# Performance work log

Measured on AMD Instinct MI355X. Metric: run time of the kernel, lower is better.

## Reference

```python
import jax, jax.numpy as jnp
import numpy as np

NUM_GRAPHS = 1024
NODES_PER_GRAPH = 1024
HIDDEN = 128
RANK_K = 8


def _mlp(x, w1, b1, w2, b2):
    # Linear -> ReLU -> Linear
    return jax.nn.relu(x @ w1 + b1) @ w2 + b2


def setup_inputs() -> dict:
    key = jax.random.key(0)
    ks = jax.random.split(key, 13)
    N = NUM_GRAPHS * NODES_PER_GRAPH
    H = jax.random.normal(ks[0], (N, HIDDEN), dtype=jnp.float32)
    # equal-size graphs: sorted graph ids 0..G-1, each repeated n_per times
    batch = jnp.repeat(jnp.arange(NUM_GRAPHS, dtype=jnp.int32), NODES_PER_GRAPH)
    s = 0.05
    p = {
        "d_w1": jax.random.normal(ks[1], (HIDDEN, HIDDEN)) * s,
        "d_b1": jnp.zeros((HIDDEN,), jnp.float32),
        "d_w2": jax.random.normal(ks[2], (HIDDEN, 2)) * s,
        "d_b2": jnp.zeros((2,), jnp.float32),
        "u_w1": jax.random.normal(ks[3], (HIDDEN, HIDDEN)) * s,
        "u_b1": jnp.zeros((HIDDEN,), jnp.float32),
        "u_w2": jax.random.normal(ks[4], (HIDDEN, 2 * RANK_K)) * s,
        "u_b2": jnp.zeros((2 * RANK_K,), jnp.float32),
        "s_w1": jax.random.normal(ks[5], (HIDDEN, HIDDEN)) * s,
        "s_b1": jnp.zeros((HIDDEN,), jnp.float32),
        "s_w2": jax.random.normal(ks[6], (HIDDEN, RANK_K)) * s,
        "s_b2": jnp.zeros((RANK_K,), jnp.float32),
    }
    return {"H": H, "batch": batch, **p}


def reference(H, batch, d_w1, d_b1, d_w2, d_b2, u_w1, u_b1, u_w2, u_b2, s_w1, s_b1, s_w2, s_b2):
    # per-node heads
    d_raw = _mlp(H, d_w1, d_b1, d_w2, d_b2)            # [N, 2]
    u_raw = _mlp(H, u_w1, u_b1, u_w2, u_b2)            # [N, 2k]
    # global_mean_pool: segment mean over graph ids
    sums = jax.ops.segment_sum(H, batch, num_segments=NUM_GRAPHS)          # [G, d]
    counts = jax.ops.segment_sum(jnp.ones((H.shape[0],), H.dtype), batch,
                                 num_segments=NUM_GRAPHS)                   # [G]
    h_pool = sums / counts[:, None]
    s_raw = _mlp(h_pool, s_w1, s_b1, s_w2, s_b2)       # [G, k]
    d_all = jax.nn.softplus(d_raw)
    s_all = jax.nn.softplus(s_raw)
    # equal-sized graphs -> the per-graph ragged gather+reshape is a pure reshape
    n = NODES_PER_GRAPH
    d = d_all.reshape(NUM_GRAPHS, 2 * n)               # per-graph d_g [2n]
    U = u_raw.reshape(NUM_GRAPHS, 2 * n, RANK_K)       # per-graph U_g [2n, k]
    return (d, U, s_all)
```

## Files before the change

kernel.cpp:

```cpp
#include <hip/hip_runtime.h>
#include <hip/hip_bf16.h>

#define G_NUM 1024
#define NPG   1024
#define HID   128
#define TILE_ROWS 32
#define TILES_PER_WG 32
#define GRAPHS_PER_WG 1

typedef __attribute__((ext_vector_type(8))) short   short8;
typedef __attribute__((ext_vector_type(4))) float   floatx4;

__device__ __forceinline__ unsigned short f2bf(float f) {
  unsigned int u = __float_as_uint(f);
  u += 0x7fffu + ((u >> 16) & 1u);
  return (unsigned short)(u >> 16);
}

__device__ __forceinline__ unsigned int cvt_pk_bf16(float lo, float hi) {
  unsigned int r;
  asm("v_cvt_pk_bf16_f32 %0, %1, %2" : "=v"(r) : "v"(lo), "v"(hi));
  return r;
}

__device__ __forceinline__ void wg_barrier_lds() {
  asm volatile("s_waitcnt lgkmcnt(0)\n\ts_barrier" ::: "memory");
}

__device__ __forceinline__ float softplusf(float x) {
  float t = exp2f(-fabsf(x) * 1.44269504f);
  return fmaxf(x, 0.f) + 0.69314718f * log2f(1.f + t);
}

__global__ void prep_kernel(const float* __restrict__ d_w1, const float* __restrict__ d_b1,
                            const float* __restrict__ d_w2,
                            const float* __restrict__ u_w1, const float* __restrict__ u_b1,
                            const float* __restrict__ u_w2,
                            const float* __restrict__ d_b2, const float* __restrict__ u_b2,
                            unsigned short* __restrict__ Wt1, unsigned short* __restrict__ W2t,
                            float* __restrict__ b1cat, float* __restrict__ b2cat)
{
  int id = blockIdx.x * blockDim.x + threadIdx.x;
  int stride = gridDim.x * blockDim.x;
  for (int idx = id; idx < 32768; idx += stride) {
    int c = idx >> 7, k = idx & 127;
    float v = (c < 128) ? d_w1[k * 128 + c] : u_w1[k * 128 + (c - 128)];
    Wt1[idx] = f2bf(v);
  }
  for (int idx = id; idx < 8192; idx += stride) {
    int c2 = idx >> 8, h = idx & 255;
    float v = 0.f;
    if (h < 128) { if (c2 < 2) v = d_w2[h * 2 + c2]; }
    else         { if (c2 >= 2 && c2 < 18) v = u_w2[(h - 128) * 16 + (c2 - 2)]; }
    W2t[idx] = f2bf(v);
  }
  for (int idx = id; idx < 256; idx += stride)
    b1cat[idx] = (idx < 128) ? d_b1[idx] : u_b1[idx - 128];
  for (int idx = id; idx < 32; idx += stride)
    b2cat[idx] = (idx < 2) ? d_b2[idx] : ((idx < 18) ? u_b2[idx - 2] : 0.f);
}

__global__ __launch_bounds__(256, 2) void fused_kernel(
    const float* __restrict__ H,
    const unsigned short* __restrict__ Wt1, const unsigned short* __restrict__ W2t,
    const float* __restrict__ b1cat, const float* __restrict__ b2cat,
    const float* __restrict__ s_w1, const float* __restrict__ s_b1,
    const float* __restrict__ s_w2, const float* __restrict__ s_b2,
    float* __restrict__ out)
{
  __shared__ __align__(16) unsigned short sH0 [TILE_ROWS * 128];
  __shared__ __align__(16) unsigned short sH1 [TILE_ROWS * 128];
  __shared__ __align__(16) unsigned short sC1a[TILE_ROWS * 256];
  __shared__ __align__(16) unsigned short sC1b[TILE_ROWS * 256];
  __shared__ __align__(16) float sX[768];

  const int tid  = threadIdx.x;
  const int g    = blockIdx.x;
  const int lane = tid & 63;
  const int w    = tid >> 6;
  const int l15  = lane & 15;
  const int l4   = lane >> 4;

  float* outD = out;
  float* outU = out + 2097152;
  float* outS = out + 18874368;

  short8 b1f[4][4];
  float  b1b[4];
#pragma unroll
  for (int nt = 0; nt < 4; ++nt) {
    int c = 64 * w + 16 * nt + l15;
    b1b[nt] = b1cat[c];
#pragma unroll
    for (int ks = 0; ks < 4; ++ks)
      b1f[nt][ks] = *(const short8*)(Wt1 + c * 128 + 32 * ks + 8 * l4);
  }
  const int r0 = 16 * (w >> 1);
  const int c0 = 16 * (w & 1);
  short8 w2f[8];
#pragma unroll
  for (int s8 = 0; s8 < 8; ++s8)
    w2f[s8] = *(const short8*)(W2t + (c0 + l15) * 256 + 32 * s8 + 8 * l4);
  const float b2v = b2cat[c0 + l15];

  const unsigned selw = (l15 & 1) ? 0x03020706u : 0x05040100u;
  const bool hi2 = (l15 & 2) != 0;

  const float* Hb = H + (long)g * (NPG * HID);

  float4 psum = make_float4(0.f, 0.f, 0.f, 0.f);

  float4 svA[4], svB[4];
#pragma unroll
  for (int i = 0; i < 4; ++i) svA[i] = *(const float4*)(Hb + i * 1024 + tid * 4);
#pragma unroll
  for (int i = 0; i < 4; ++i) svB[i] = *(const float4*)(Hb + 4096 + i * 1024 + tid * 4);

  auto regionC = [&](const unsigned short* sCr, int tc) {
    floatx4 acc2 = {b2v, b2v, b2v, b2v};
#pragma unroll
    for (int s8 = 0; s8 < 8; ++s8) {
      int r = r0 + l15;
      int bo = r * 512 + 64 * s8 + 16 * l4;
      bo ^= (r & 7) << 4;
      short8 a2 = *(const short8*)((const char*)sCr + bo);
      acc2 = __builtin_amdgcn_mfma_f32_16x16x32_bf16(a2, w2f[s8], acc2, 0, 0, 0);
    }
    long nodebase = (long)g * NPG + tc * TILE_ROWS + r0 + 4 * l4;
    if (c0 == 0) {
#pragma unroll
      for (int q = 0; q < 4; ++q) {
        float v = acc2[q];
        long node = nodebase + q;
        if (l15 < 2) outD[node * 2 + l15] = softplusf(v);
        else         outU[node * 16 + (l15 - 2)] = v;
      }
    } else {
#pragma unroll
      for (int q = 0; q < 4; ++q) {
        long node = nodebase + q;
        if (l15 < 2) outU[node * 16 + 14 + l15] = acc2[q];
      }
    }
  };

  auto body = [&](float4 (&cur)[4], unsigned short* sHw,
                  const unsigned short* sCr, unsigned short* sCw, int t) {
#pragma unroll
    for (int i = 0; i < 4; ++i) {
      float4 v = cur[i];
      psum.x += v.x; psum.y += v.y; psum.z += v.z; psum.w += v.w;
      int row = i * 8 + (tid >> 5);
      int bo = row * 256 + (tid & 31) * 8;
      bo ^= (row & 7) << 4;
      uint2 p;
      p.x = cvt_pk_bf16(v.x, v.y);
      p.y = cvt_pk_bf16(v.z, v.w);
      *(uint2*)((char*)sHw + bo) = p;
    }
    if (t + 2 < TILES_PER_WG) {
      const float* nb = Hb + (t + 2) * (TILE_ROWS * HID);
#pragma unroll
      for (int i = 0; i < 4; ++i) cur[i] = *(const float4*)(nb + i * 1024 + tid * 4);
    }
    wg_barrier_lds();

    if (t > 0) regionC(sCr, t - 1);

    floatx4 acc[2][4];
#pragma unroll
    for (int mt = 0; mt < 2; ++mt)
#pragma unroll
      for (int nt = 0; nt < 4; ++nt)
        acc[mt][nt] = (floatx4){b1b[nt], b1b[nt], b1b[nt], b1b[nt]};

#pragma unroll
    for (int ks = 0; ks < 4; ++ks) {
      short8 a[2];
#pragma unroll
      for (int mt = 0; mt < 2; ++mt) {
        int row = 16 * mt + l15;
        int bo = row * 256 + 64 * ks + 16 * l4;
        bo ^= (row & 7) << 4;
        a[mt] = *(const short8*)((const char*)sHw + bo);
      }
#pragma unroll
      for (int mt = 0; mt < 2; ++mt)
#pragma unroll
        for (int nt = 0; nt < 4; ++nt)
          acc[mt][nt] = __builtin_amdgcn_mfma_f32_16x16x32_bf16(a[mt], b1f[nt][ks], acc[mt][nt], 0, 0, 0);
    }

#pragma unroll
    for (int mt = 0; mt < 2; ++mt) {
#pragma unroll
      for (int nt = 0; nt < 4; ++nt) {
        float v0 = fmaxf(acc[mt][nt][0], 0.f);
        float v1 = fmaxf(acc[mt][nt][1], 0.f);
        float v2 = fmaxf(acc[mt][nt][2], 0.f);
        float v3 = fmaxf(acc[mt][nt][3], 0.f);
        unsigned A = cvt_pk_bf16(v0, v1);
        unsigned B = cvt_pk_bf16(v2, v3);
        unsigned An = (unsigned)__builtin_amdgcn_mov_dpp((int)A, 0xB1, 0xF, 0xF, true);
        unsigned Bn = (unsigned)__builtin_amdgcn_mov_dpp((int)B, 0xB1, 0xF, 0xF, true);
        unsigned WA = __builtin_amdgcn_perm(An, A, selw);
        unsigned WB = __builtin_amdgcn_perm(Bn, B, selw);
        unsigned WAs = (unsigned)__builtin_amdgcn_mov_dpp((int)WA, 0x4E, 0xF, 0xF, true);
        unsigned WBs = (unsigned)__builtin_amdgcn_mov_dpp((int)WB, 0x4E, 0xF, 0xF, true);
        uint2 o;
        o.x = hi2 ? WBs : WA;
        o.y = hi2 ? WB  : WAs;
        int row = 16 * mt + 4 * l4 + (l15 & 3);
        int cb  = 64 * w + 16 * nt + (l15 & 12);
        int bo = row * 512 + cb * 2;
        bo ^= (row & 7) << 4;
        *(uint2*)((char*)sCw + bo) = o;
      }
    }
  };

  for (int t = 0; t < TILES_PER_WG; t += 2) {
    body(svA, sH0, sC1b, sC1a, t);
    body(svB, sH1, sC1a, sC1b, t + 1);
  }
  wg_barrier_lds();
  regionC(sC1b, TILES_PER_WG - 1);

  {
    float4 p = psum;
    __syncthreads();
    p.x += __shfl_xor(p.x, 32);
    p.y += __shfl_xor(p.y, 32);
    p.z += __shfl_xor(p.z, 32);
    p.w += __shfl_xor(p.w, 32);
    if (lane < 32) *(float4*)&sX[w * 128 + lane * 4] = p;
    __syncthreads();
    if (tid < 128) {
      float pc = sX[tid] + sX[128 + tid] + sX[256 + tid] + sX[384 + tid];
      sX[512 + tid] = pc;
    }
    __syncthreads();
    if (tid < 128) {
      float a = s_b1[tid];
      const float inv = 1.f / 1024.f;
#pragma unroll 8
      for (int k = 0; k < 128; ++k)
        a = fmaf(sX[512 + k] * inv, s_w1[k * 128 + tid], a);
      sX[640 + tid] = fmaxf(a, 0.f);
    }
    __syncthreads();
    if (tid < 8) {
      float a = s_b2[tid];
#pragma unroll 8
      for (int h = 0; h < 128; ++h)
        a = fmaf(sX[640 + h], s_w2[h * 8 + tid], a);
      outS[(long)g * 8 + tid] = softplusf(a);
    }
  }
}

extern "C" void kernel_launch(void* const* d_in, const int* in_sizes, int n_in,
                              void* d_out, int out_size, void* d_ws, size_t ws_size,
                              hipStream_t stream)
{
  const float* H    = (const float*)d_in[0];
  const float* d_w1 = (const float*)d_in[2];
  const float* d_b1 = (const float*)d_in[3];
  const float* d_w2 = (const float*)d_in[4];
  const float* d_b2 = (const float*)d_in[5];
  const float* u_w1 = (const float*)d_in[6];
  const float* u_b1 = (const float*)d_in[7];
  const float* u_w2 = (const float*)d_in[8];
  const float* u_b2 = (const float*)d_in[9];
  const float* s_w1 = (const float*)d_in[10];
  const float* s_b1 = (const float*)d_in[11];
  const float* s_w2 = (const float*)d_in[12];
  const float* s_b2 = (const float*)d_in[13];

  unsigned short* Wt1   = (unsigned short*)d_ws;
  unsigned short* W2t   = (unsigned short*)((char*)d_ws + 65536);
  float*          b1cat = (float*)((char*)d_ws + 81920);
  float*          b2cat = (float*)((char*)d_ws + 82944);

  hipLaunchKernelGGL(prep_kernel, dim3(64), dim3(256), 0, stream,
                     d_w1, d_b1, d_w2, u_w1, u_b1, u_w2, d_b2, u_b2,
                     Wt1, W2t, b1cat, b2cat);

  hipLaunchKernelGGL(fused_kernel, dim3(G_NUM), dim3(256), 0, stream,
                     H, Wt1, W2t, b1cat, b2cat, s_w1, s_b1, s_w2, s_b2,
                     (float*)d_out);
}
```

Measured before the change: 181.0 us.

## Split each graph across two workgroups and move pooled head to separate kernel

Halves rows per workgroup so the fused MLP kernel launches 2048 workgroups instead of 1024, giving finer load balance across the CUs. Each workgroup writes a partial column sum to a workspace buffer. A new small kernel combines the two partials per graph, then runs the pooled MLP and softplus. This adds an extra launch, a workspace round trip, and more per-workgroup prologue overhead (weight fragment loads) in exchange for better occupancy and tail balance.

```diff
diff --git a/kernel.cpp b/kernel.cpp
--- a/kernel.cpp
+++ b/kernel.cpp
@@ -5,8 +5,8 @@
 #define NPG   1024
 #define HID   128
 #define TILE_ROWS 32
-#define TILES_PER_WG 32
-#define GRAPHS_PER_WG 1
+#define TILES_PER_WG 16
+#define ROWS_PER_WG 512
 
 typedef __attribute__((ext_vector_type(8))) short   short8;
 typedef __attribute__((ext_vector_type(4))) float   floatx4;
@@ -64,8 +64,7 @@
     const float* __restrict__ H,
     const unsigned short* __restrict__ Wt1, const unsigned short* __restrict__ W2t,
     const float* __restrict__ b1cat, const float* __restrict__ b2cat,
-    const float* __restrict__ s_w1, const float* __restrict__ s_b1,
-    const float* __restrict__ s_w2, const float* __restrict__ s_b2,
+    float* __restrict__ pws,
     float* __restrict__ out)
 {
   __shared__ __align__(16) unsigned short sH0 [TILE_ROWS * 128];
@@ -75,7 +74,7 @@
   __shared__ __align__(16) float sX[768];
 
   const int tid  = threadIdx.x;
-  const int g    = blockIdx.x;
+  const int bid  = blockIdx.x;
   const int lane = tid & 63;
   const int w    = tid >> 6;
   const int l15  = lane & 15;
@@ -83,7 +82,6 @@
 
   float* outD = out;
   float* outU = out + 2097152;
-  float* outS = out + 18874368;
 
   short8 b1f[4][4];
   float  b1b[4];
@@ -106,7 +104,7 @@
   const unsigned selw = (l15 & 1) ? 0x03020706u : 0x05040100u;
   const bool hi2 = (l15 & 2) != 0;
 
-  const float* Hb = H + (long)g * (NPG * HID);
+  const float* Hb = H + (long)bid * (ROWS_PER_WG * HID);
 
   float4 psum = make_float4(0.f, 0.f, 0.f, 0.f);
 
@@ -126,7 +124,7 @@
       short8 a2 = *(const short8*)((const char*)sCr + bo);
       acc2 = __builtin_amdgcn_mfma_f32_16x16x32_bf16(a2, w2f[s8], acc2, 0, 0, 0);
     }
-    long nodebase = (long)g * NPG + tc * TILE_ROWS + r0 + 4 * l4;
+    long nodebase = (long)bid * ROWS_PER_WG + tc * TILE_ROWS + r0 + 4 * l4;
     if (c0 == 0) {
 #pragma unroll
       for (int q = 0; q < 4; ++q) {
@@ -237,25 +235,34 @@
     __syncthreads();
     if (tid < 128) {
       float pc = sX[tid] + sX[128 + tid] + sX[256 + tid] + sX[384 + tid];
-      sX[512 + tid] = pc;
-    }
-    __syncthreads();
-    if (tid < 128) {
-      float a = s_b1[tid];
-      const float inv = 1.f / 1024.f;
+      pws[(long)bid * 128 + tid] = pc;
+    }
+  }
+}
+
+__global__ __launch_bounds__(128) void shead_kernel(
+    const float* __restrict__ pws,
+    const float* __restrict__ s_w1, const float* __restrict__ s_b1,
+    const float* __restrict__ s_w2, const float* __restrict__ s_b2,
+    float* __restrict__ outS)
+{
+  __shared__ float pool[128];
+  __shared__ float hid[128];
+  const int g = blockIdx.x, tid = threadIdx.x;
+  pool[tid] = (pws[(long)(2 * g) * 128 + tid] + pws[(long)(2 * g + 1) * 128 + tid]) * (1.f / 1024.f);
+  __syncthreads();
+  float a = s_b1[tid];
 #pragma unroll 8
-      for (int k = 0; k < 128; ++k)
-        a = fmaf(sX[512 + k] * inv, s_w1[k * 128 + tid], a);
-      sX[640 + tid] = fmaxf(a, 0.f);
-    }
-    __syncthreads();
-    if (tid < 8) {
-      float a = s_b2[tid];
+  for (int k = 0; k < 128; ++k)
+    a = fmaf(pool[k], s_w1[k * 128 + tid], a);
+  hid[tid] = fmaxf(a, 0.f);
+  __syncthreads();
+  if (tid < 8) {
+    float b = s_b2[tid];
 #pragma unroll 8
-      for (int h = 0; h < 128; ++h)
-        a = fmaf(sX[640 + h], s_w2[h * 8 + tid], a);
-      outS[(long)g * 8 + tid] = softplusf(a);
-    }
+    for (int h = 0; h < 128; ++h)
+      b = fmaf(hid[h], s_w2[h * 8 + tid], b);
+    outS[(long)g * 8 + tid] = softplusf(b);
   }
 }
 
@@ -281,12 +288,16 @@
   unsigned short* W2t   = (unsigned short*)((char*)d_ws + 65536);
   float*          b1cat = (float*)((char*)d_ws + 81920);
   float*          b2cat = (float*)((char*)d_ws + 82944);
+  float*          pws   = (float*)((char*)d_ws + 86016);
 
   hipLaunchKernelGGL(prep_kernel, dim3(64), dim3(256), 0, stream,
                      d_w1, d_b1, d_w2, u_w1, u_b1, u_w2, d_b2, u_b2,
                      Wt1, W2t, b1cat, b2cat);
 
-  hipLaunchKernelGGL(fused_kernel, dim3(G_NUM), dim3(256), 0, stream,
-                     H, Wt1, W2t, b1cat, b2cat, s_w1, s_b1, s_w2, s_b2,
-                     (float*)d_out);
-}
+  hipLaunchKernelGGL(fused_kernel, dim3(2048), dim3(256), 0, stream,
+                     H, Wt1, W2t, b1cat, b2cat, pws, (float*)d_out);
+
+  hipLaunchKernelGGL(shead_kernel, dim3(G_NUM), dim3(128), 0, stream,
+                     pws, s_w1, s_b1, s_w2, s_b2,
+                     (float*)d_out + 18874368);
+}
```

Result: slower. 195.6 us (+8.1%).
